# Kernel optimization log

Measured on AMD Instinct MI355X. Metric: run time of the kernel, lower is better.

## Reference

```python
import jax, jax.numpy as jnp
import numpy as np

N_NODES = 50000
N_EDGES = 800000
N_FEAT = 512
N_HID = 256
N_LAYER = 4
N_CLASS = 40


def setup_inputs() -> dict:
    key = jax.random.key(0)
    ks = jax.random.split(key, 16)
    x = jax.random.normal(ks[0], (N_NODES, N_FEAT), dtype=jnp.float32)
    edge_index = jax.random.randint(ks[1], (2, N_EDGES), 0, N_NODES, dtype=jnp.int64 if jax.config.jax_enable_x64 else jnp.int32)

    def glorot(k, fan_in, fan_out):
        lim = np.sqrt(6.0 / (fan_in + fan_out)).astype(np.float32)
        return jax.random.uniform(k, (fan_in, fan_out), jnp.float32, -lim, lim)

    in_gc_W = glorot(ks[2], N_FEAT, N_HID)
    in_gc_b = jnp.zeros((N_HID,), jnp.float32)
    in_lin_W = glorot(ks[3], N_FEAT, N_HID)
    in_lin_b = jnp.zeros((N_HID,), jnp.float32)
    # n_layer-1 = 3 hidden conv / lin pairs, stacked on leading axis
    convs_W = jnp.stack([glorot(jax.random.fold_in(ks[4], i), N_HID, N_HID) for i in range(N_LAYER - 1)])
    convs_b = jnp.zeros((N_LAYER - 1, N_HID), jnp.float32)
    lins_W = jnp.stack([glorot(jax.random.fold_in(ks[5], i), N_HID, N_HID) for i in range(N_LAYER - 1)])
    lins_b = jnp.zeros((N_LAYER - 1, N_HID), jnp.float32)
    out_W = glorot(ks[6], N_HID * N_LAYER, N_CLASS)
    out_b = jnp.zeros((N_CLASS,), jnp.float32)
    return {
        "x": x, "edge_index": edge_index,
        "in_gc_W": in_gc_W, "in_gc_b": in_gc_b,
        "in_lin_W": in_lin_W, "in_lin_b": in_lin_b,
        "convs_W": convs_W, "convs_b": convs_b,
        "lins_W": lins_W, "lins_b": lins_b,
        "out_W": out_W, "out_b": out_b,
    }


def reference(x, edge_index, in_gc_W, in_gc_b, in_lin_W, in_lin_b,
              convs_W, convs_b, lins_W, lins_b, out_W, out_b):
    src, dst = edge_index[0], edge_index[1]
    n = x.shape[0]
    # GCN symmetric normalization with self-loops: deg = 1 + in-degree
    deg = jnp.zeros((n,), jnp.float32).at[dst].add(1.0) + 1.0
    dinv = jax.lax.rsqrt(deg)
    edge_norm = dinv[src] * dinv[dst]        # [E]
    self_norm = dinv * dinv                  # [N]

    def gcn(h, W, b):
        hw = h @ W                           # [N, out]
        msg = hw[src] * edge_norm[:, None]   # gather + scale
        agg = jax.ops.segment_sum(msg, dst, num_segments=n)
        agg = agg + hw * self_norm[:, None]  # self-loop term
        return agg + b

    # inductive: GCNConv + linear residual; dropout = identity (eval mode)
    h = jax.nn.relu(gcn(x, in_gc_W, in_gc_b) + x @ in_lin_W + in_lin_b)
    xs = [h]
    for i in range(convs_W.shape[0]):
        h = jax.nn.relu(gcn(h, convs_W[i], convs_b[i]) + h @ lins_W[i] + lins_b[i])
        xs.append(h)
    # JumpingKnowledge mode='cat'
    jk = jnp.concatenate(xs, axis=-1)        # [N, n_hid * n_layer]
    return jk @ out_W + out_b
```

## Files before the change

### kernel.cpp

```cpp
#include <hip/hip_runtime.h>

typedef _Float16 half8 __attribute__((ext_vector_type(8)));
typedef _Float16 half4 __attribute__((ext_vector_type(4)));
typedef float floatx4 __attribute__((ext_vector_type(4)));

__global__ __launch_bounds__(256) void zero_i32(int* __restrict__ p, int n) {
    int i = blockIdx.x * 256 + threadIdx.x;
    if (i < n) p[i] = 0;
}

__global__ __launch_bounds__(256) void hist_dst(const int* __restrict__ dst,
                                                int* __restrict__ count, int E) {
    int e = blockIdx.x * 256 + threadIdx.x;
    if (e < E) atomicAdd(&count[dst[e]], 1);
}

__global__ __launch_bounds__(256) void make_dinv(const int* __restrict__ count,
                                                 float* __restrict__ dinv, int n) {
    int i = blockIdx.x * 256 + threadIdx.x;
    if (i < n) dinv[i] = rsqrtf(1.0f + (float)count[i]);
}

__global__ __launch_bounds__(256) void cast_f32_f16(const float* __restrict__ in,
                                                    _Float16* __restrict__ out, int n4) {
    int i = blockIdx.x * 256 + threadIdx.x;
    if (i < n4) {
        float4 v = *(const float4*)&in[(size_t)i * 4];
        half4 h = { (_Float16)v.x, (_Float16)v.y, (_Float16)v.z, (_Float16)v.w };
        *(half4*)&out[(size_t)i * 4] = h;
    }
}

__global__ __launch_bounds__(256) void transpose_cast(const float* __restrict__ W,
                                                      _Float16* __restrict__ WT,
                                                      int K, int N) {
    int k = blockIdx.x;
    int n = threadIdx.x;
    if (n < N) WT[(size_t)n * K + k] = (_Float16)W[(size_t)k * N + n];
}

__global__ __launch_bounds__(256) void scan_block(const int* __restrict__ count,
                                                  int* __restrict__ incl,
                                                  int* __restrict__ blocksum, int n) {
    __shared__ int tmp[256];
    int t = threadIdx.x;
    int i = blockIdx.x * 256 + t;
    int v = (i < n) ? count[i] : 0;
    tmp[t] = v;
    __syncthreads();
    for (int off = 1; off < 256; off <<= 1) {
        int x = (t >= off) ? tmp[t - off] : 0;
        __syncthreads();
        tmp[t] += x;
        __syncthreads();
    }
    if (i < n) incl[i] = tmp[t];
    if (t == 255) blocksum[blockIdx.x] = tmp[255];
}

__global__ __launch_bounds__(256) void scan_top(const int* __restrict__ blocksum,
                                                int* __restrict__ blockoff, int nb) {
    __shared__ int tmp[256];
    int t = threadIdx.x;
    int v = (t < nb) ? blocksum[t] : 0;
    tmp[t] = v;
    __syncthreads();
    for (int off = 1; off < 256; off <<= 1) {
        int x = (t >= off) ? tmp[t - off] : 0;
        __syncthreads();
        tmp[t] += x;
        __syncthreads();
    }
    if (t < nb) blockoff[t] = tmp[t] - v;
}

__global__ __launch_bounds__(256) void make_rowptr(const int* __restrict__ incl,
                                                   const int* __restrict__ count,
                                                   const int* __restrict__ blockoff,
                                                   int* __restrict__ rowptr,
                                                   int* __restrict__ cursor, int n) {
    int i = blockIdx.x * 256 + threadIdx.x;
    if (i < n) {
        int r = incl[i] - count[i] + blockoff[blockIdx.x];
        rowptr[i] = r;
        cursor[i] = r;
    }
}

__global__ __launch_bounds__(256) void scatter_perm(const int* __restrict__ src,
                                                    const int* __restrict__ dst,
                                                    const float* __restrict__ dinv,
                                                    int* __restrict__ cursor,
                                                    int* __restrict__ sorted_src,
                                                    float* __restrict__ sorted_norm, int E) {
    int e = blockIdx.x * 256 + threadIdx.x;
    if (e < E) {
        int d = dst[e], s = src[e];
        int slot = atomicAdd(&cursor[d], 1);
        sorted_src[slot] = s;
        sorted_norm[slot] = dinv[s] * dinv[d];
    }
}

#define GBM 128
#define GBK 64
#define LSTR 72

__global__ __launch_bounds__(256) void gemm_f16(
    const _Float16* __restrict__ A, int lda,
    const _Float16* __restrict__ BT,
    const float* __restrict__ bias0,
    const float* __restrict__ bias1,
    float* __restrict__ Cf, _Float16* __restrict__ Ch, int ldc,
    int M, int N, int K)
{
    __shared__ _Float16 As[GBM * LSTR];
    __shared__ _Float16 Bs[GBM * LSTR];

    const int tid  = threadIdx.x;
    const int wave = tid >> 6;
    const int lane = tid & 63;
    const int q    = lane >> 4;
    const int r    = lane & 15;

    const int wm = (wave & 1) * 64;
    const int wn = (wave >> 1) * 64;

    const int bm = blockIdx.x * GBM;
    const int bn = blockIdx.y * GBM;

    floatx4 acc[4][4] = {};

    for (int k0 = 0; k0 < K; k0 += GBK) {
        #pragma unroll
        for (int i = 0; i < 4; ++i) {
            int c = tid + i * 256;
            int row = c >> 3;
            int koff = (c & 7) * 8;
            {
                int gm = bm + row; if (gm > M - 1) gm = M - 1;
                uint4 v = *(const uint4*)&A[(size_t)gm * lda + k0 + koff];
                *(uint4*)&As[row * LSTR + koff] = v;
            }
            {
                int gn = bn + row; if (gn > N - 1) gn = N - 1;
                uint4 v = *(const uint4*)&BT[(size_t)gn * K + k0 + koff];
                *(uint4*)&Bs[row * LSTR + koff] = v;
            }
        }
        __syncthreads();

        #pragma unroll
        for (int kk = 0; kk < 2; ++kk) {
            half8 af[4], bf[4];
            #pragma unroll
            for (int mi = 0; mi < 4; ++mi)
                af[mi] = *(const half8*)&As[(wm + mi * 16 + r) * LSTR + kk * 32 + q * 8];
            #pragma unroll
            for (int ni = 0; ni < 4; ++ni)
                bf[ni] = *(const half8*)&Bs[(wn + ni * 16 + r) * LSTR + kk * 32 + q * 8];
            #pragma unroll
            for (int mi = 0; mi < 4; ++mi)
                #pragma unroll
                for (int ni = 0; ni < 4; ++ni)
                    acc[mi][ni] = __builtin_amdgcn_mfma_f32_16x16x32_f16(
                        af[mi], bf[ni], acc[mi][ni], 0, 0, 0);
        }
        __syncthreads();
    }

    #pragma unroll
    for (int mi = 0; mi < 4; ++mi) {
        #pragma unroll
        for (int ni = 0; ni < 4; ++ni) {
            int col = bn + wn + ni * 16 + r;
            if (col >= N) continue;
            float badd = 0.0f;
            if (bias0) badd += bias0[col];
            if (bias1) badd += bias1[col];
            #pragma unroll
            for (int reg = 0; reg < 4; ++reg) {
                int gm = bm + wm + mi * 16 + q * 4 + reg;
                if (gm >= M) continue;
                float v = acc[mi][ni][reg] + badd;
                if (Ch) Ch[(size_t)gm * ldc + col] = (_Float16)v;
                else    Cf[(size_t)gm * ldc + col] = v;
            }
        }
    }
}

__global__ __launch_bounds__(256) void aggregate_csr(
    const int* __restrict__ rowptr, const int* __restrict__ count,
    const int* __restrict__ sorted_src, const float* __restrict__ sorted_norm,
    const float* __restrict__ dinv,
    const _Float16* __restrict__ hw,
    const float* __restrict__ lin,
    _Float16* __restrict__ jk_col,
    int n)
{
    int wave = (blockIdx.x * 256 + threadIdx.x) >> 6;
    int lane = threadIdx.x & 63;
    if (wave >= n) return;
    const int i = wave;

    const int start = rowptr[i];
    const int deg   = count[i];

    float4 acc = *(const float4*)&lin[(size_t)i * 256 + lane * 4];

    for (int base = 0; base < deg; base += 64) {
        int m = deg - base;
        if (m > 64) m = 64;
        int   s_l  = 0;
        float nm_l = 0.0f;
        if (lane < m) {
            s_l  = sorted_src[start + base + lane];
            nm_l = sorted_norm[start + base + lane];
        }
        for (int j = 0; j < m; ++j) {
            int   s  = __shfl(s_l, j, 64);
            float nm = __shfl(nm_l, j, 64);
            half4 h = *(const half4*)&hw[(size_t)s * 256 + lane * 4];
            acc.x = fmaf((float)h[0], nm, acc.x);
            acc.y = fmaf((float)h[1], nm, acc.y);
            acc.z = fmaf((float)h[2], nm, acc.z);
            acc.w = fmaf((float)h[3], nm, acc.w);
        }
    }

    float di = dinv[i];
    float sn = di * di;
    half4 hs = *(const half4*)&hw[(size_t)i * 256 + lane * 4];
    acc.x = fmaxf(fmaf((float)hs[0], sn, acc.x), 0.0f);
    acc.y = fmaxf(fmaf((float)hs[1], sn, acc.y), 0.0f);
    acc.z = fmaxf(fmaf((float)hs[2], sn, acc.z), 0.0f);
    acc.w = fmaxf(fmaf((float)hs[3], sn, acc.w), 0.0f);

    half4 o = { (_Float16)acc.x, (_Float16)acc.y, (_Float16)acc.z, (_Float16)acc.w };
    *(half4*)&jk_col[(size_t)i * 1024 + lane * 4] = o;
}

extern "C" void kernel_launch(void* const* d_in, const int* in_sizes, int n_in,
                              void* d_out, int out_size, void* d_ws, size_t ws_size,
                              hipStream_t stream) {
    const float* x        = (const float*)d_in[0];
    const int*   ei       = (const int*)d_in[1];
    const float* in_gc_W  = (const float*)d_in[2];
    const float* in_gc_b  = (const float*)d_in[3];
    const float* in_lin_W = (const float*)d_in[4];
    const float* in_lin_b = (const float*)d_in[5];
    const float* convs_W  = (const float*)d_in[6];
    const float* convs_b  = (const float*)d_in[7];
    const float* lins_W   = (const float*)d_in[8];
    const float* lins_b   = (const float*)d_in[9];
    const float* out_W    = (const float*)d_in[10];
    const float* out_b    = (const float*)d_in[11];

    const int N = 50000;
    const int E = in_sizes[1] / 2;
    const int F = 512, H = 256, L = 4, NC = 40;

    const int* src = ei;
    const int* dst = ei + E;

    char* ws = (char*)d_ws;
    auto carve = [&](size_t bytes) { void* p = ws; ws += (bytes + 255) & ~(size_t)255; return p; };
    float*    dinv       = (float*)carve((size_t)N * 4);
    int*      count      = (int*)  carve((size_t)N * 4);
    int*      incl       = (int*)  carve((size_t)N * 4);
    int*      rowptr     = (int*)  carve((size_t)N * 4);
    int*      cursor     = (int*)  carve((size_t)N * 4);
    int*      blocksum   = (int*)  carve(256 * 4);
    int*      blockoff   = (int*)  carve(256 * 4);
    int*      sorted_src = (int*)  carve((size_t)E * 4);
    float*    sorted_nrm = (float*)carve((size_t)E * 4);
    _Float16* xh         = (_Float16*)carve((size_t)N * F * 2);
    _Float16* gcWT0      = (_Float16*)carve((size_t)H * F * 2);
    _Float16* liWT0      = (_Float16*)carve((size_t)H * F * 2);
    _Float16* gcWT       = (_Float16*)carve((size_t)3 * H * H * 2);
    _Float16* liWT       = (_Float16*)carve((size_t)3 * H * H * 2);
    _Float16* outWT      = (_Float16*)carve((size_t)NC * H * L * 2);
    float*    lin        = (float*)   carve((size_t)N * H * 4);
    _Float16* hw         = (_Float16*)carve((size_t)N * H * 2);
    _Float16* jk_h       = (_Float16*)carve((size_t)N * H * L * 2);
    float*    out        = (float*)d_out;

    const int nbN = (N + 255) / 256;
    const int nbE = (E + 255) / 256;

    zero_i32<<<nbN, 256, 0, stream>>>(count, N);
    hist_dst<<<nbE, 256, 0, stream>>>(dst, count, E);
    make_dinv<<<nbN, 256, 0, stream>>>(count, dinv, N);
    scan_block<<<nbN, 256, 0, stream>>>(count, incl, blocksum, N);
    scan_top<<<1, 256, 0, stream>>>(blocksum, blockoff, nbN);
    make_rowptr<<<nbN, 256, 0, stream>>>(incl, count, blockoff, rowptr, cursor, N);
    scatter_perm<<<nbE, 256, 0, stream>>>(src, dst, dinv, cursor, sorted_src, sorted_nrm, E);

    cast_f32_f16<<<(N * F / 4 + 255) / 256, 256, 0, stream>>>(x, xh, N * F / 4);
    transpose_cast<<<F, 256, 0, stream>>>(in_gc_W,  gcWT0, F, H);
    transpose_cast<<<F, 256, 0, stream>>>(in_lin_W, liWT0, F, H);
    for (int l = 0; l < 3; ++l) {
        transpose_cast<<<H, 256, 0, stream>>>(convs_W + (size_t)l * H * H, gcWT + (size_t)l * H * H, H, H);
        transpose_cast<<<H, 256, 0, stream>>>(lins_W  + (size_t)l * H * H, liWT + (size_t)l * H * H, H, H);
    }
    transpose_cast<<<H * L, 256, 0, stream>>>(out_W, outWT, H * L, NC);

    const dim3 ggrid((N + GBM - 1) / GBM, H / GBM);
    const dim3 ogrid((N + GBM - 1) / GBM, 1);
    const int agg_blocks = (N + 3) / 4;

    for (int l = 0; l < L; ++l) {
        const _Float16* Ah = (l == 0) ? xh : (jk_h + (size_t)(l - 1) * H);
        int lda            = (l == 0) ? F : H * L;
        int K              = (l == 0) ? F : H;
        const _Float16* gT = (l == 0) ? gcWT0 : (gcWT + (size_t)(l - 1) * H * H);
        const _Float16* lT = (l == 0) ? liWT0 : (liWT + (size_t)(l - 1) * H * H);
        const float* gcB   = (l == 0) ? in_gc_b  : (convs_b + (size_t)(l - 1) * H);
        const float* liB   = (l == 0) ? in_lin_b : (lins_b  + (size_t)(l - 1) * H);

        gemm_f16<<<ggrid, 256, 0, stream>>>(Ah, lda, lT, liB, gcB, lin, nullptr, H, N, H, K);
        gemm_f16<<<ggrid, 256, 0, stream>>>(Ah, lda, gT, nullptr, nullptr, nullptr, hw, H, N, H, K);
        aggregate_csr<<<agg_blocks, 256, 0, stream>>>(rowptr, count, sorted_src, sorted_nrm,
                                                      dinv, hw, lin, jk_h + (size_t)l * H, N);
    }

    gemm_f16<<<ogrid, 256, 0, stream>>>(jk_h, H * L, outWT, out_b, nullptr,
                                        out, nullptr, NC, N, NC, H * L);
}
```

Before: 841.9 us.

## Fuse lin and GCN GEMMs, use direct-to-LDS swizzled loads, fp16 lin, unrolled gather

Measured after the change: 746.5 us. 1.13x faster.

```diff
diff --git a/kernel.cpp b/kernel.cpp
--- a/kernel.cpp
+++ b/kernel.cpp
@@ -3,6 +3,13 @@
 typedef _Float16 half8 __attribute__((ext_vector_type(8)));
 typedef _Float16 half4 __attribute__((ext_vector_type(4)));
 typedef float floatx4 __attribute__((ext_vector_type(4)));
+
+__device__ __forceinline__ void gld16(const _Float16* g, _Float16* lds_base) {
+    __builtin_amdgcn_global_load_lds(
+        (const __attribute__((address_space(1))) unsigned int*)g,
+        (__attribute__((address_space(3))) unsigned int*)lds_base,
+        16, 0, 0);
+}
 
 __global__ __launch_bounds__(256) void zero_i32(int* __restrict__ p, int n) {
     int i = blockIdx.x * 256 + threadIdx.x;
@@ -102,20 +109,17 @@
     }
 }
 
-#define GBM 128
-#define GBK 64
-#define LSTR 72
-
-__global__ __launch_bounds__(256) void gemm_f16(
+template<bool DUAL>
+__global__ __launch_bounds__(256) void gemm_mfma(
     const _Float16* __restrict__ A, int lda,
-    const _Float16* __restrict__ BT,
-    const float* __restrict__ bias0,
-    const float* __restrict__ bias1,
-    float* __restrict__ Cf, _Float16* __restrict__ Ch, int ldc,
-    int M, int N, int K)
+    const _Float16* __restrict__ BT, int Nrows,
+    const float* __restrict__ bias0, const float* __restrict__ bias1,
+    _Float16* __restrict__ lin_h, _Float16* __restrict__ hw,
+    float* __restrict__ Cf, int ldc,
+    int M, int K)
 {
-    __shared__ _Float16 As[GBM * LSTR];
-    __shared__ _Float16 Bs[GBM * LSTR];
+    __shared__ _Float16 As[128 * 64];
+    __shared__ _Float16 Bs[128 * 64];
 
     const int tid  = threadIdx.x;
     const int wave = tid >> 6;
@@ -126,39 +130,37 @@
     const int wm = (wave & 1) * 64;
     const int wn = (wave >> 1) * 64;
 
-    const int bm = blockIdx.x * GBM;
-    const int bn = blockIdx.y * GBM;
+    const int bn = blockIdx.x * 128;
+    const int bm = blockIdx.y * 128;
+
+    const int srow  = wave * 32;
+    const int lrow8 = lane >> 3;
+    const int cp    = lane & 7;
 
     floatx4 acc[4][4] = {};
 
-    for (int k0 = 0; k0 < K; k0 += GBK) {
+    for (int k0 = 0; k0 < K; k0 += 64) {
         #pragma unroll
-        for (int i = 0; i < 4; ++i) {
-            int c = tid + i * 256;
-            int row = c >> 3;
-            int koff = (c & 7) * 8;
-            {
-                int gm = bm + row; if (gm > M - 1) gm = M - 1;
-                uint4 v = *(const uint4*)&A[(size_t)gm * lda + k0 + koff];
-                *(uint4*)&As[row * LSTR + koff] = v;
-            }
-            {
-                int gn = bn + row; if (gn > N - 1) gn = N - 1;
-                uint4 v = *(const uint4*)&BT[(size_t)gn * K + k0 + koff];
-                *(uint4*)&Bs[row * LSTR + koff] = v;
-            }
+        for (int t = 0; t < 4; ++t) {
+            int lrow = srow + t * 8 + lrow8;
+            int c    = cp ^ (lrow & 7);
+            int gm = bm + lrow; if (gm > M - 1) gm = M - 1;
+            gld16(&A[(size_t)gm * lda + k0 + c * 8], &As[(srow + t * 8) * 64]);
+            int gn = bn + lrow; if (gn > Nrows - 1) gn = Nrows - 1;
+            gld16(&BT[(size_t)gn * K + k0 + c * 8], &Bs[(srow + t * 8) * 64]);
         }
         __syncthreads();
 
         #pragma unroll
         for (int kk = 0; kk < 2; ++kk) {
+            const int sc = ((kk << 2) | q) ^ (r & 7);
             half8 af[4], bf[4];
             #pragma unroll
             for (int mi = 0; mi < 4; ++mi)
-                af[mi] = *(const half8*)&As[(wm + mi * 16 + r) * LSTR + kk * 32 + q * 8];
+                af[mi] = *(const half8*)&As[(wm + mi * 16 + r) * 64 + sc * 8];
             #pragma unroll
             for (int ni = 0; ni < 4; ++ni)
-                bf[ni] = *(const half8*)&Bs[(wn + ni * 16 + r) * LSTR + kk * 32 + q * 8];
+                bf[ni] = *(const half8*)&Bs[(wn + ni * 16 + r) * 64 + sc * 8];
             #pragma unroll
             for (int mi = 0; mi < 4; ++mi)
                 #pragma unroll
@@ -169,23 +171,37 @@
         __syncthreads();
     }
 
-    #pragma unroll
-    for (int mi = 0; mi < 4; ++mi) {
+    if (DUAL) {
+        const bool islin = (bn < 256);
+        _Float16* dstp = islin ? lin_h : hw;
         #pragma unroll
         for (int ni = 0; ni < 4; ++ni) {
             int col = bn + wn + ni * 16 + r;
-            if (col >= N) continue;
-            float badd = 0.0f;
-            if (bias0) badd += bias0[col];
-            if (bias1) badd += bias1[col];
-            #pragma unroll
-            for (int reg = 0; reg < 4; ++reg) {
-                int gm = bm + wm + mi * 16 + q * 4 + reg;
-                if (gm >= M) continue;
-                float v = acc[mi][ni][reg] + badd;
-                if (Ch) Ch[(size_t)gm * ldc + col] = (_Float16)v;
-                else    Cf[(size_t)gm * ldc + col] = v;
-            }
+            int c2  = islin ? col : col - 256;
+            float badd = islin ? (bias0[col] + bias1[col]) : 0.0f;
+            #pragma unroll
+            for (int mi = 0; mi < 4; ++mi)
+                #pragma unroll
+                for (int reg = 0; reg < 4; ++reg) {
+                    int gm = bm + wm + mi * 16 + q * 4 + reg;
+                    if (gm < M)
+                        dstp[(size_t)gm * 256 + c2] = (_Float16)(acc[mi][ni][reg] + badd);
+                }
+        }
+    } else {
+        #pragma unroll
+        for (int ni = 0; ni < 4; ++ni) {
+            int col = bn + wn + ni * 16 + r;
+            if (col >= Nrows) continue;
+            float badd = bias0 ? bias0[col] : 0.0f;
+            #pragma unroll
+            for (int mi = 0; mi < 4; ++mi)
+                #pragma unroll
+                for (int reg = 0; reg < 4; ++reg) {
+                    int gm = bm + wm + mi * 16 + q * 4 + reg;
+                    if (gm < M)
+                        Cf[(size_t)gm * ldc + col] = acc[mi][ni][reg] + badd;
+                }
         }
     }
 }
@@ -195,9 +211,8 @@
     const int* __restrict__ sorted_src, const float* __restrict__ sorted_norm,
     const float* __restrict__ dinv,
     const _Float16* __restrict__ hw,
-    const float* __restrict__ lin,
-    _Float16* __restrict__ jk_col,
-    int n)
+    const _Float16* __restrict__ lin_h,
+    _Float16* __restrict__ jk_col, int n)
 {
     int wave = (blockIdx.x * 256 + threadIdx.x) >> 6;
     int lane = threadIdx.x & 63;
@@ -207,7 +222,8 @@
     const int start = rowptr[i];
     const int deg   = count[i];
 
-    float4 acc = *(const float4*)&lin[(size_t)i * 256 + lane * 4];
+    half4 l4 = *(const half4*)&lin_h[(size_t)i * 256 + lane * 4];
+    float4 acc = make_float4((float)l4[0], (float)l4[1], (float)l4[2], (float)l4[3]);
 
     for (int base = 0; base < deg; base += 64) {
         int m = deg - base;
@@ -218,14 +234,24 @@
             s_l  = sorted_src[start + base + lane];
             nm_l = sorted_norm[start + base + lane];
         }
-        for (int j = 0; j < m; ++j) {
-            int   s  = __shfl(s_l, j, 64);
-            float nm = __shfl(nm_l, j, 64);
-            half4 h = *(const half4*)&hw[(size_t)s * 256 + lane * 4];
-            acc.x = fmaf((float)h[0], nm, acc.x);
-            acc.y = fmaf((float)h[1], nm, acc.y);
-            acc.z = fmaf((float)h[2], nm, acc.z);
-            acc.w = fmaf((float)h[3], nm, acc.w);
+        for (int j = 0; j < m; j += 4) {
+            half4 hv[4];
+            float nm[4];
+            #pragma unroll
+            for (int k2 = 0; k2 < 4; ++k2) {
+                int jj  = j + k2;
+                int idx = (jj < m) ? jj : (m - 1);
+                int s   = __shfl(s_l, idx, 64);
+                nm[k2]  = (jj < m) ? __shfl(nm_l, jj, 64) : 0.0f;
+                hv[k2]  = *(const half4*)&hw[(size_t)s * 256 + lane * 4];
+            }
+            #pragma unroll
+            for (int k2 = 0; k2 < 4; ++k2) {
+                acc.x = fmaf((float)hv[k2][0], nm[k2], acc.x);
+                acc.y = fmaf((float)hv[k2][1], nm[k2], acc.y);
+                acc.z = fmaf((float)hv[k2][2], nm[k2], acc.z);
+                acc.w = fmaf((float)hv[k2][3], nm[k2], acc.w);
+            }
         }
     }
 
@@ -276,12 +302,10 @@
     int*      sorted_src = (int*)  carve((size_t)E * 4);
     float*    sorted_nrm = (float*)carve((size_t)E * 4);
     _Float16* xh         = (_Float16*)carve((size_t)N * F * 2);
-    _Float16* gcWT0      = (_Float16*)carve((size_t)H * F * 2);
-    _Float16* liWT0      = (_Float16*)carve((size_t)H * F * 2);
-    _Float16* gcWT       = (_Float16*)carve((size_t)3 * H * H * 2);
-    _Float16* liWT       = (_Float16*)carve((size_t)3 * H * H * 2);
+    _Float16* w0comb     = (_Float16*)carve((size_t)512 * F * 2);
+    _Float16* wcomb      = (_Float16*)carve((size_t)3 * 512 * H * 2);
     _Float16* outWT      = (_Float16*)carve((size_t)NC * H * L * 2);
-    float*    lin        = (float*)   carve((size_t)N * H * 4);
+    _Float16* lin_h      = (_Float16*)carve((size_t)N * H * 2);
     _Float16* hw         = (_Float16*)carve((size_t)N * H * 2);
     _Float16* jk_h       = (_Float16*)carve((size_t)N * H * L * 2);
     float*    out        = (float*)d_out;
@@ -298,33 +322,33 @@
     scatter_perm<<<nbE, 256, 0, stream>>>(src, dst, dinv, cursor, sorted_src, sorted_nrm, E);
 
     cast_f32_f16<<<(N * F / 4 + 255) / 256, 256, 0, stream>>>(x, xh, N * F / 4);
-    transpose_cast<<<F, 256, 0, stream>>>(in_gc_W,  gcWT0, F, H);
-    transpose_cast<<<F, 256, 0, stream>>>(in_lin_W, liWT0, F, H);
+    transpose_cast<<<F, 256, 0, stream>>>(in_lin_W, w0comb,               F, H);
+    transpose_cast<<<F, 256, 0, stream>>>(in_gc_W,  w0comb + (size_t)H * F, F, H);
     for (int l = 0; l < 3; ++l) {
-        transpose_cast<<<H, 256, 0, stream>>>(convs_W + (size_t)l * H * H, gcWT + (size_t)l * H * H, H, H);
-        transpose_cast<<<H, 256, 0, stream>>>(lins_W  + (size_t)l * H * H, liWT + (size_t)l * H * H, H, H);
+        _Float16* wl = wcomb + (size_t)l * 512 * H;
+        transpose_cast<<<H, 256, 0, stream>>>(lins_W  + (size_t)l * H * H, wl,                   H, H);
+        transpose_cast<<<H, 256, 0, stream>>>(convs_W + (size_t)l * H * H, wl + (size_t)H * H,   H, H);
     }
     transpose_cast<<<H * L, 256, 0, stream>>>(out_W, outWT, H * L, NC);
 
-    const dim3 ggrid((N + GBM - 1) / GBM, H / GBM);
-    const dim3 ogrid((N + GBM - 1) / GBM, 1);
+    const dim3 dgrid(4, (N + 127) / 128);
+    const dim3 ogrid(1, (N + 127) / 128);
     const int agg_blocks = (N + 3) / 4;
 
     for (int l = 0; l < L; ++l) {
         const _Float16* Ah = (l == 0) ? xh : (jk_h + (size_t)(l - 1) * H);
         int lda            = (l == 0) ? F : H * L;
         int K              = (l == 0) ? F : H;
-        const _Float16* gT = (l == 0) ? gcWT0 : (gcWT + (size_t)(l - 1) * H * H);
-        const _Float16* lT = (l == 0) ? liWT0 : (liWT + (size_t)(l - 1) * H * H);
+        const _Float16* BT = (l == 0) ? w0comb : (wcomb + (size_t)(l - 1) * 512 * H);
         const float* gcB   = (l == 0) ? in_gc_b  : (convs_b + (size_t)(l - 1) * H);
         const float* liB   = (l == 0) ? in_lin_b : (lins_b  + (size_t)(l - 1) * H);
 
-        gemm_f16<<<ggrid, 256, 0, stream>>>(Ah, lda, lT, liB, gcB, lin, nullptr, H, N, H, K);
-        gemm_f16<<<ggrid, 256, 0, stream>>>(Ah, lda, gT, nullptr, nullptr, nullptr, hw, H, N, H, K);
+        gemm_mfma<true><<<dgrid, 256, 0, stream>>>(Ah, lda, BT, 512, liB, gcB,
+                                                   lin_h, hw, nullptr, 0, N, K);
         aggregate_csr<<<agg_blocks, 256, 0, stream>>>(rowptr, count, sorted_src, sorted_nrm,
-                                                      dinv, hw, lin, jk_h + (size_t)l * H, N);
-    }
-
-    gemm_f16<<<ogrid, 256, 0, stream>>>(jk_h, H * L, outWT, out_b, nullptr,
-                                        out, nullptr, NC, N, NC, H * L);
-}
+                                                      dinv, hw, lin_h, jk_h + (size_t)l * H, N);
+    }
+
+    gemm_mfma<false><<<ogrid, 256, 0, stream>>>(jk_h, H * L, outWT, NC, out_b, nullptr,
+                                                nullptr, nullptr, out, NC, N, H * L);
+}
```
